# Optimization experiments

Hardware: AMD Instinct MI355X
Metric: run time of the kernel (lower is better)

## Reference

```python
import jax, jax.numpy as jnp
import numpy as np

D_K = 64
NEG = -1000000000.0

def setup_inputs() -> dict:
    key = jax.random.key(0)
    kq, kk, kv, km = jax.random.split(key, 4)
    B, H, S = 2, 16, 2048
    query = jax.random.normal(kq, (B, H, S, D_K), dtype=jnp.float32)
    k_ = jax.random.normal(kk, (B, H, S, D_K), dtype=jnp.float32)
    value = jax.random.normal(kv, (B, H, S, D_K), dtype=jnp.float32)
    mask = jax.random.randint(km, (1, 1, S, S), 0, 2, dtype=jnp.int32)
    return {"query": query, "key": k_, "value": value, "mask": mask}

def reference(query, key, value, mask):
    # scores: [B,H,S,S]
    scale = jnp.asarray(D_K ** 0.5, dtype=query.dtype)
    scores = jnp.einsum('bhqd,bhkd->bhqk', query, key) / scale
    scores = jnp.where(mask == 0, jnp.asarray(NEG, dtype=scores.dtype), scores)
    proba = jax.nn.softmax(scores, axis=-1)
    return jnp.einsum('bhqk,bhkd->bhqd', proba, value)
```

## Files before the change

### kernel.cpp

```cpp
#include <hip/hip_runtime.h>
#include <hip/hip_bf16.h>
#include <stdint.h>


#define SLEN 2048
#define DK 64
#define KVB 64
#define NT (SLEN / KVB)
#define QTILE 256
#define MFIX 13.0f

typedef __attribute__((ext_vector_type(8)))  short    short8;
typedef __attribute__((ext_vector_type(4)))  short    s4v;
typedef __attribute__((ext_vector_type(16))) float    f32x16;
typedef __attribute__((ext_vector_type(4)))  float    float4v;
typedef __attribute__((ext_vector_type(4)))  unsigned uint4v;
typedef __attribute__((ext_vector_type(4)))  int      int4v;

static __device__ __forceinline__ float fexp2(float x){
#if __has_builtin(__builtin_amdgcn_exp2f)
  return __builtin_amdgcn_exp2f(x);
#else
  float r; asm("v_exp_f32 %0, %1" : "=v"(r) : "v"(x)); return r;
#endif
}
static __device__ __forceinline__ unsigned short f2bfu(float x){
  __hip_bfloat16 h = __float2bfloat16(x);
  return __builtin_bit_cast(unsigned short, h);
}
static __device__ __forceinline__ unsigned pkbf(float lo, float hi){
  return (unsigned)f2bfu(lo) | ((unsigned)f2bfu(hi) << 16);
}
static __device__ __forceinline__ short8 pack8s(float4v a, float4v b, float s){
  short8 r;
  r[0]=(short)f2bfu(a[0]*s); r[1]=(short)f2bfu(a[1]*s);
  r[2]=(short)f2bfu(a[2]*s); r[3]=(short)f2bfu(a[3]*s);
  r[4]=(short)f2bfu(b[0]*s); r[5]=(short)f2bfu(b[1]*s);
  r[6]=(short)f2bfu(b[2]*s); r[7]=(short)f2bfu(b[3]*s);
  return r;
}

__global__ void ScaledDotAttention_mask_pack(const int* __restrict__ mask,
                                             uint32_t* __restrict__ mtw){
  int lane = threadIdx.x & 63;
  int wid  = threadIdx.x >> 6;
  int q    = blockIdx.x * 4 + wid;
  const int* row = mask + (size_t)q * SLEN;
  #pragma unroll 4
  for (int i = 0; i < 32; ++i){
    unsigned long long b = __ballot(row[i*64 + lane] != 0);
    if (lane == 0)
      *(unsigned long long*)(mtw + (size_t)i*4096 + (size_t)q*2) = b;
  }
}

template<bool USE_WS>
__global__ __launch_bounds__(512, 2)
void ScaledDotAttention_attn(const float* __restrict__ Q, const float* __restrict__ K,
                             const float* __restrict__ V, const uint32_t* __restrict__ mtw,
                             const int* __restrict__ mask, float* __restrict__ Out)
{
  __shared__ alignas(16) unsigned short Kl[KVB*DK];
  __shared__ alignas(16) unsigned short Vt[DK*KVB];

  const int tid  = threadIdx.x;
  const int lane = tid & 63;
  const int l31  = lane & 31;
  const int hi   = lane >> 5;
  const int wid  = __builtin_amdgcn_readfirstlane(tid >> 6);

  const int bid = blockIdx.x;
  const int xcd = bid & 7, ii = bid >> 3;
  const int bh  = xcd + 8*(ii & 3);
  const int qt  = ii >> 2;

  const float* Qb = Q + (size_t)bh*SLEN*DK;
  const float* Kb = K + (size_t)bh*SLEN*DK;
  const float* Vb = V + (size_t)bh*SLEN*DK;

  const int qbase = qt*QTILE + wid*32;
  const float C1 = 0.18033688011112042592f;

  short8 qf[4];
  {
    const float* qrow = Qb + (size_t)(qbase + l31)*DK + hi*8;
    #pragma unroll
    for (int c = 0; c < 4; ++c){
      float4v f0 = *(const float4v*)(qrow + c*16);
      float4v f1 = *(const float4v*)(qrow + c*16 + 4);
      qf[c] = pack8s(f0, f1, C1);
    }
  }

  f32x16 O0, O1;
  #pragma unroll
  for (int r = 0; r < 16; ++r){ O0[r] = 0.f; O1[r] = 0.f; }
  float lsum = 0.f;
  const float vneg = -1.0e9f;

  const int skr  = tid >> 3;
  const int sc8b = tid & 7;
  float4v ka0, ka1, va0, va1;

  auto LOADT = [&](int it){
    const float* kp = Kb + (size_t)it*KVB*DK + skr*DK + sc8b*8;
    ka0 = *(const float4v*)kp;  ka1 = *(const float4v*)(kp + 4);
    const float* vp = Vb + (size_t)it*KVB*DK + skr*DK + sc8b*8;
    va0 = *(const float4v*)vp;  va1 = *(const float4v*)(vp + 4);
  };

  LOADT(0);

  #pragma unroll 1
  for (int it = 0; it < NT; ++it){
    __syncthreads();
    {
      short8 kw = pack8s(ka0, ka1, 1.0f);
      int kaddr = (skr*128 + sc8b*16) ^ ((skr & 7) << 4);
      *(short8*)((char*)Kl + kaddr) = kw;
      unsigned short vs[8];
      vs[0]=f2bfu(va0[0]); vs[1]=f2bfu(va0[1]); vs[2]=f2bfu(va0[2]); vs[3]=f2bfu(va0[3]);
      vs[4]=f2bfu(va1[0]); vs[5]=f2bfu(va1[1]); vs[6]=f2bfu(va1[2]); vs[7]=f2bfu(va1[3]);
      #pragma unroll
      for (int j = 0; j < 8; ++j){
        int d = sc8b*8 + j;
        int vaddr = (d*128 + skr*2) ^ ((d & 15) << 3);
        *(unsigned short*)((char*)Vt + vaddr) = vs[j];
      }
    }
    __syncthreads();
    if (it + 1 < NT) LOADT(it + 1);

    uint64_t wv = 0;
    if constexpr (USE_WS){
      wv = *(const uint64_t*)(mtw + (size_t)it*4096 + (size_t)(qbase + l31)*2);
    }

    #pragma unroll
    for (int ks = 0; ks < 2; ++ks){
      f32x16 acc;
      #pragma unroll
      for (int r = 0; r < 16; ++r) acc[r] = -MFIX;
      #pragma unroll
      for (int dc = 0; dc < 4; ++dc){
        int kaddr = ((ks*32 + l31)*128 + dc*32 + hi*16) ^ ((l31 & 7) << 4);
        short8 kf = *(const short8*)((const char*)Kl + kaddr);
        acc = __builtin_amdgcn_mfma_f32_32x32x16_bf16(kf, qf[dc], acc, 0, 0, 0);
      }
      float p[16];
      if constexpr (USE_WS){
        uint32_t w = (uint32_t)(wv >> (32*ks)) >> (4*hi);
        #pragma unroll
        for (int r = 0; r < 16; ++r){
          unsigned bit = (w >> ((r & 3) + 8*(r >> 2))) & 1u;
          p[r] = fexp2(bit ? acc[r] : vneg);
        }
      } else {
        const int* mri = mask + (size_t)(qbase + l31)*SLEN + it*KVB + ks*32 + 4*hi;
        int4v g0 = *(const int4v*)(mri);
        int4v g1 = *(const int4v*)(mri + 8);
        int4v g2 = *(const int4v*)(mri + 16);
        int4v g3 = *(const int4v*)(mri + 24);
        #pragma unroll
        for (int r = 0; r < 16; ++r){
          int gi = r >> 2;
          int gv = (gi==0 ? g0[r&3] : gi==1 ? g1[r&3] : gi==2 ? g2[r&3] : g3[r&3]);
          p[r] = fexp2(gv ? acc[r] : vneg);
        }
      }
      float q0 = (p[0]+p[1]) + (p[2]+p[3]);
      float q1 = (p[4]+p[5]) + (p[6]+p[7]);
      float q2 = (p[8]+p[9]) + (p[10]+p[11]);
      float q3 = (p[12]+p[13]) + (p[14]+p[15]);
      lsum += (q0+q1) + (q2+q3);

      #pragma unroll
      for (int kc = 0; kc < 2; ++kc){
        unsigned pw0 = pkbf(p[8*kc+0], p[8*kc+1]);
        unsigned pw1 = pkbf(p[8*kc+2], p[8*kc+3]);
        unsigned pw2 = pkbf(p[8*kc+4], p[8*kc+5]);
        unsigned pw3 = pkbf(p[8*kc+6], p[8*kc+7]);
        uint4v pw; pw[0]=pw0; pw[1]=pw1; pw[2]=pw2; pw[3]=pw3;
        short8 pf = __builtin_bit_cast(short8, pw);
        int kbyte = (ks*32 + kc*16 + 4*hi) * 2;
        #pragma unroll
        for (int hf = 0; hf < 2; ++hf){
          int d = hf*32 + l31;
          int rowb = d*128;
          int swz = (d & 15) << 3;
          s4v a = *(const s4v*)((const char*)Vt + ((rowb + kbyte) ^ swz));
          s4v b = *(const s4v*)((const char*)Vt + ((rowb + kbyte + 16) ^ swz));
          short8 vf;
          #pragma unroll
          for (int j = 0; j < 4; ++j){ vf[j] = a[j]; vf[4+j] = b[j]; }
          if (hf == 0) O0 = __builtin_amdgcn_mfma_f32_32x32x16_bf16(vf, pf, O0, 0, 0, 0);
          else         O1 = __builtin_amdgcn_mfma_f32_32x32x16_bf16(vf, pf, O1, 0, 0, 0);
        }
      }
    }
  }

  float lt = lsum + __shfl_xor(lsum, 32, 64);
  float rinv = 1.0f / lt;
  float* orow = Out + ((size_t)bh*SLEN + qbase + l31)*DK;
  #pragma unroll
  for (int r = 0; r < 16; ++r){
    int c0 = (r & 3) + 8*(r >> 2) + 4*hi;
    orow[c0]      = O0[r] * rinv;
    orow[c0 + 32] = O1[r] * rinv;
  }
}

extern "C" void kernel_launch(void* const* d_in, const int* in_sizes, int n_in,
                              void* d_out, int out_size, void* d_ws, size_t ws_size,
                              hipStream_t stream) {
  const float* Q    = (const float*)d_in[0];
  const float* K    = (const float*)d_in[1];
  const float* V    = (const float*)d_in[2];
  const int*   mask = (const int*)d_in[3];
  float* Out = (float*)d_out;

  if (ws_size >= (size_t)(SLEN/64) * SLEN * 2 * sizeof(uint32_t)) {
    uint32_t* mtw = (uint32_t*)d_ws;
    ScaledDotAttention_mask_pack<<<dim3(SLEN/4), dim3(256), 0, stream>>>(mask, mtw);
    ScaledDotAttention_attn<true><<<dim3(256), dim3(512), 0, stream>>>(Q, K, V, mtw, mask, Out);
  } else {
    ScaledDotAttention_attn<false><<<dim3(256), dim3(512), 0, stream>>>(Q, K, V, (const uint32_t*)nullptr, mask, Out);
  }
}
```

Before: 86.46 us.

## Double-buffer K/V LDS tiles and transpose V via padded 2x4 gathers

```diff
diff --git a/kernel.cpp b/kernel.cpp
--- a/kernel.cpp
+++ b/kernel.cpp
@@ -9,11 +9,14 @@
 #define NT (SLEN / KVB)
 #define QTILE 256
 #define MFIX 13.0f
+#define VPB 136
 
 typedef __attribute__((ext_vector_type(8)))  short    short8;
 typedef __attribute__((ext_vector_type(4)))  short    s4v;
+typedef __attribute__((ext_vector_type(4)))  unsigned short us4;
 typedef __attribute__((ext_vector_type(16))) float    f32x16;
 typedef __attribute__((ext_vector_type(4)))  float    float4v;
+typedef __attribute__((ext_vector_type(2)))  float    float2v;
 typedef __attribute__((ext_vector_type(4)))  unsigned uint4v;
 typedef __attribute__((ext_vector_type(4)))  int      int4v;
 
@@ -60,8 +63,8 @@
                              const float* __restrict__ V, const uint32_t* __restrict__ mtw,
                              const int* __restrict__ mask, float* __restrict__ Out)
 {
-  __shared__ alignas(16) unsigned short Kl[KVB*DK];
-  __shared__ alignas(16) unsigned short Vt[DK*KVB];
+  __shared__ alignas(16) unsigned short Kl[2][KVB*64];
+  __shared__ alignas(16) unsigned short Vt[2][DK*(VPB/2)];
 
   const int tid  = threadIdx.x;
   const int lane = tid & 63;
@@ -100,41 +103,50 @@
 
   const int skr  = tid >> 3;
   const int sc8b = tid & 7;
-  float4v ka0, ka1, va0, va1;
+  const int vd   = (tid & 31) * 2;
+  const int vk   = (tid >> 5) * 4;
+  float4v ka0, ka1;
+  float2v vv0, vv1, vv2, vv3;
 
   auto LOADT = [&](int it){
     const float* kp = Kb + (size_t)it*KVB*DK + skr*DK + sc8b*8;
     ka0 = *(const float4v*)kp;  ka1 = *(const float4v*)(kp + 4);
-    const float* vp = Vb + (size_t)it*KVB*DK + skr*DK + sc8b*8;
-    va0 = *(const float4v*)vp;  va1 = *(const float4v*)(vp + 4);
+    const float* vp = Vb + (size_t)it*KVB*DK + vk*DK + vd;
+    vv0 = *(const float2v*)vp;
+    vv1 = *(const float2v*)(vp + DK);
+    vv2 = *(const float2v*)(vp + 2*DK);
+    vv3 = *(const float2v*)(vp + 3*DK);
   };
 
+  auto WRITE = [&](int buf){
+    short8 kw = pack8s(ka0, ka1, 1.0f);
+    int kaddr = (skr*128 + sc8b*16) ^ ((skr & 7) << 4);
+    *(short8*)((char*)&Kl[buf][0] + kaddr) = kw;
+    us4 r0, r1;
+    r0[0]=f2bfu(vv0[0]); r0[1]=f2bfu(vv1[0]); r0[2]=f2bfu(vv2[0]); r0[3]=f2bfu(vv3[0]);
+    r1[0]=f2bfu(vv0[1]); r1[1]=f2bfu(vv1[1]); r1[2]=f2bfu(vv2[1]); r1[3]=f2bfu(vv3[1]);
+    *(us4*)((char*)&Vt[buf][0] + vd*VPB + vk*2)       = r0;
+    *(us4*)((char*)&Vt[buf][0] + (vd+1)*VPB + vk*2)   = r1;
+  };
+
   LOADT(0);
+  WRITE(0);
+  LOADT(1);
+  __syncthreads();
+  int cur = 0;
 
   #pragma unroll 1
   for (int it = 0; it < NT; ++it){
-    __syncthreads();
-    {
-      short8 kw = pack8s(ka0, ka1, 1.0f);
-      int kaddr = (skr*128 + sc8b*16) ^ ((skr & 7) << 4);
-      *(short8*)((char*)Kl + kaddr) = kw;
-      unsigned short vs[8];
-      vs[0]=f2bfu(va0[0]); vs[1]=f2bfu(va0[1]); vs[2]=f2bfu(va0[2]); vs[3]=f2bfu(va0[3]);
-      vs[4]=f2bfu(va1[0]); vs[5]=f2bfu(va1[1]); vs[6]=f2bfu(va1[2]); vs[7]=f2bfu(va1[3]);
-      #pragma unroll
-      for (int j = 0; j < 8; ++j){
-        int d = sc8b*8 + j;
-        int vaddr = (d*128 + skr*2) ^ ((d & 15) << 3);
-        *(unsigned short*)((char*)Vt + vaddr) = vs[j];
-      }
-    }
-    __syncthreads();
-    if (it + 1 < NT) LOADT(it + 1);
+    if (it + 1 < NT) WRITE(cur ^ 1);
+    if (it + 2 < NT) LOADT(it + 2);
 
     uint64_t wv = 0;
     if constexpr (USE_WS){
       wv = *(const uint64_t*)(mtw + (size_t)it*4096 + (size_t)(qbase + l31)*2);
     }
+
+    const unsigned short* Klc = &Kl[cur][0];
+    const unsigned short* Vtc = &Vt[cur][0];
 
     #pragma unroll
     for (int ks = 0; ks < 2; ++ks){
@@ -144,7 +156,7 @@
       #pragma unroll
       for (int dc = 0; dc < 4; ++dc){
         int kaddr = ((ks*32 + l31)*128 + dc*32 + hi*16) ^ ((l31 & 7) << 4);
-        short8 kf = *(const short8*)((const char*)Kl + kaddr);
+        short8 kf = *(const short8*)((const char*)Klc + kaddr);
         acc = __builtin_amdgcn_mfma_f32_32x32x16_bf16(kf, qf[dc], acc, 0, 0, 0);
       }
       float p[16];
@@ -186,10 +198,9 @@
         #pragma unroll
         for (int hf = 0; hf < 2; ++hf){
           int d = hf*32 + l31;
-          int rowb = d*128;
-          int swz = (d & 15) << 3;
-          s4v a = *(const s4v*)((const char*)Vt + ((rowb + kbyte) ^ swz));
-          s4v b = *(const s4v*)((const char*)Vt + ((rowb + kbyte + 16) ^ swz));
+          int base = d*VPB + kbyte;
+          s4v a = *(const s4v*)((const char*)Vtc + base);
+          s4v b = *(const s4v*)((const char*)Vtc + base + 16);
           short8 vf;
           #pragma unroll
           for (int j = 0; j < 4; ++j){ vf[j] = a[j]; vf[4+j] = b[j]; }
@@ -198,6 +209,9 @@
         }
       }
     }
+
+    __syncthreads();
+    cur ^= 1;
   }
 
   float lt = lsum + __shfl_xor(lsum, 32, 64);
```

Result: faster. 79.41 us (-8.1%).
